# Performance work log

Hardware: AMD Instinct MI355X
Metric: run time of the kernel (lower is better)

## Reference

```python
import jax, jax.numpy as jnp
import numpy as np

B, Q, D, H, EF = 64, 300, 512, 8, 4
DH = D // H            # 64, per-head dim for scores
DV = (D * EF) // H     # 256, per-head value dim


def setup_inputs() -> dict:
    key = jax.random.key(0)
    ks = jax.random.split(key, 10)
    s = 0.02
    return {
        "query_feats": jax.random.normal(ks[0], (B, Q, D), jnp.float32),
        "bias": jax.random.normal(ks[1], (1, H, Q, Q), jnp.float32),
        "W_gen": jax.random.normal(ks[2], (D, D), jnp.float32) * s,
        "b_gen": jax.random.normal(ks[3], (D,), jnp.float32) * s,
        "W_val": jax.random.normal(ks[4], (D, D * EF), jnp.float32) * s,
        "b_val": jax.random.normal(ks[5], (D * EF,), jnp.float32) * s,
        "W_out": jax.random.normal(ks[6], (D * EF, D), jnp.float32) * s,
        "b_out": jax.random.normal(ks[7], (D,), jnp.float32) * s,
        "weight_bank": jnp.ones((1, H, Q, Q), jnp.float32) / np.sqrt(DH).astype(np.float32),
    }


def reference(query_feats, bias, W_gen, b_gen, W_val, b_val, W_out, b_out, weight_bank):
    bs, nq, d = query_feats.shape
    h = weight_bank.shape[1]
    # params_generator -> dynamic mixing matrix M: [bs, h, dh, nq]
    M = (query_feats @ W_gen + b_gen).reshape(bs, nq, h, -1).transpose(0, 2, 3, 1)
    # value: [bs, h, nq, dv]
    value = (query_feats @ W_val + b_val).reshape(bs, nq, h, -1).transpose(0, 2, 1, 3)
    # queries split per head: [bs, h, nq, dh]
    q = query_feats.reshape(bs, nq, h, -1).transpose(0, 2, 1, 3)
    # scores: [bs, h, nq, nq], scaled by learned weight bank + bias, GELU (exact), softmax
    scores = jnp.einsum('bhqd,bhdk->bhqk', q, M) * weight_bank + bias
    attn = jax.nn.softmax(jax.nn.gelu(scores, approximate=False), axis=-1)
    out = jnp.einsum('bhqk,bhkv->bhqv', attn, value)
    out = out.transpose(0, 2, 1, 3).reshape(bs, nq, -1)
    out = out @ W_out + b_out
    return out + query_feats
```

## Files before the change

### kernel.cpp

```cpp
#include <hip/hip_runtime.h>
#include <hip/hip_bf16.h>

typedef __attribute__((ext_vector_type(4))) float f32x4;
typedef __attribute__((ext_vector_type(8))) short s16x8;
typedef __attribute__((ext_vector_type(4))) short s16x4;

#define MFMA16(A, B, C) __builtin_amdgcn_mfma_f32_16x16x32_bf16((A), (B), (C), 0, 0, 0)

#define GLDS16(gsrc, ldst) __builtin_amdgcn_global_load_lds(                   \
    (const __attribute__((address_space(1))) void*)(gsrc),                    \
    (__attribute__((address_space(3))) void*)(ldst), 16, 0, 0)

__device__ __forceinline__ ushort f2bf(float f) {
    __hip_bfloat16 h = __float2bfloat16(f);
    return *reinterpret_cast<ushort*>(&h);
}

__device__ __forceinline__ float gelu_exact(float x) {
    float z = 0.70710678118f * x;
    float az = fabsf(z);
    float t = 1.0f / fmaf(0.3275911f, az, 1.0f);
    float poly = t * (0.254829592f + t * (-0.284496736f + t * (1.421413741f +
                 t * (-1.453152027f + t * 1.061405429f))));
    float e = __expf(-az * az);
    float erfv = copysignf(1.0f - poly * e, z);
    return 0.5f * x * (1.0f + erfv);
}

__global__ __launch_bounds__(256) void k_prep(const float* __restrict__ qf,
                                              ushort* __restrict__ qf_bf,
                                              const float* __restrict__ W_gen,
                                              const float* __restrict__ W_val,
                                              const float* __restrict__ W_out,
                                              ushort* __restrict__ WgvT,
                                              ushort* __restrict__ WoT,
                                              ushort* __restrict__ Vt) {
    __shared__ float tile[32][33];
    int blk = blockIdx.x;
    if (blk < 9600) {
        int i = (blk * 256 + threadIdx.x) * 4;
        float4 v = *(const float4*)(qf + i);
        ushort4 o;
        o.x = f2bf(v.x); o.y = f2bf(v.y); o.z = f2bf(v.z); o.w = f2bf(v.w);
        *(ushort4*)(qf_bf + i) = o;
        return;
    }
    blk -= 9600;
    if (blk >= 2304) {
        int i = ((blk - 2304) * 256 + threadIdx.x) * 8;
        int bh = i >> 13, within = i & 8191;
        s16x8 z = {0, 0, 0, 0, 0, 0, 0, 0};
        *(s16x8*)(Vt + ((size_t)bh * 10 + 9) * 8192 + within) = z;
        return;
    }
    const float* w; ushort* wt; int K, N, kx, ny;
    if (blk < 256)       { w = W_gen; wt = WgvT;             K = 512;  N = 512;
                           kx = blk & 15;          ny = blk >> 4; }
    else if (blk < 1280) { w = W_val; wt = WgvT + 512 * 512; K = 512;  N = 2048;
                           int b2 = blk - 256;  kx = b2 & 15; ny = b2 >> 4; }
    else                 { w = W_out; wt = WoT;              K = 2048; N = 512;
                           int b2 = blk - 1280; kx = b2 & 63; ny = b2 >> 6; }
    int k0 = kx * 32, n0 = ny * 32;
    int tx = threadIdx.x & 31, ty = threadIdx.x >> 5;
    #pragma unroll
    for (int i = ty; i < 32; i += 8)
        tile[i][tx] = w[(size_t)(k0 + i) * N + n0 + tx];
    __syncthreads();
    #pragma unroll
    for (int i = ty; i < 32; i += 8)
        wt[(size_t)(n0 + i) * K + k0 + tx] = f2bf(tile[tx][i]);
}

template <int OUT>
__global__ __launch_bounds__(512, 2) void k_gemm256(const ushort* __restrict__ A,
                                                    const ushort* __restrict__ BT,
                                                    const float* __restrict__ b1,
                                                    const float* __restrict__ b2,
                                                    void* __restrict__ o1,
                                                    void* __restrict__ o2,
                                                    int K, int GY) {
    __shared__ __align__(16) ushort As[2][256 * 64];
    __shared__ __align__(16) ushort Bs[2][256 * 64];
    int id = blockIdx.x;
    int xcd = id & 7, s = id >> 3;
    int mxl = s / GY, ny = s - mxl * GY;
    int mx = xcd * 10 + mxl;
    if (mx >= 75) return;
    int m0 = mx * 256, n0g = ny * 256;

    int t = threadIdx.x, l = t & 63, w = t >> 6;
    int wr = w >> 2, wc = w & 3;
    int lr = l & 15, lg = l >> 4;

    int rsrc[4], ksrc[4];
    #pragma unroll
    for (int c8 = 0; c8 < 4; ++c8) {
        int o = (c8 * 512 + t) * 16;
        int op = o ^ (((o >> 7) & 7) << 4);
        rsrc[c8] = op >> 7;
        ksrc[c8] = (op & 127) >> 1;
    }

    auto stage = [&](int kt, int buf) {
        int k0 = kt * 64;
        ushort* AsB = &As[buf][0];
        ushort* BsB = &Bs[buf][0];
        #pragma unroll
        for (int c8 = 0; c8 < 4; ++c8) {
            int dst = (c8 * 512 + w * 64) * 8;
            GLDS16(A  + (size_t)(m0 + rsrc[c8]) * K + k0 + ksrc[c8], AsB + dst);
            GLDS16(BT + (size_t)(n0g + rsrc[c8]) * K + k0 + ksrc[c8], BsB + dst);
        }
    };

    f32x4 acc[8][4];
    #pragma unroll
    for (int i = 0; i < 8; ++i)
        #pragma unroll
        for (int j = 0; j < 4; ++j)
            acc[i][j] = (f32x4){0.f, 0.f, 0.f, 0.f};

    int NT = K >> 6;
    stage(0, 0);
    stage(1, 1);

    for (int kt = 0; kt < NT; ++kt) {
        if (kt + 1 < NT) asm volatile("s_waitcnt vmcnt(8)" ::: "memory");
        else             asm volatile("s_waitcnt vmcnt(0)" ::: "memory");
        __builtin_amdgcn_s_barrier();

        int cur = kt & 1;
        const char* Ab = (const char*)&As[cur][0];
        const char* Bb = (const char*)&Bs[cur][0];
        #pragma unroll
        for (int ks = 0; ks < 2; ++ks) {
            int kb = (ks * 64 + lg * 16) ^ ((lr & 7) << 4);
            s16x8 af[8], bfv[4];
            #pragma unroll
            for (int rt = 0; rt < 8; ++rt)
                af[rt] = *(const s16x8*)(Ab + (wr * 128 + rt * 16 + lr) * 128 + kb);
            #pragma unroll
            for (int ct = 0; ct < 4; ++ct)
                bfv[ct] = *(const s16x8*)(Bb + (wc * 64 + ct * 16 + lr) * 128 + kb);
            #pragma unroll
            for (int rt = 0; rt < 8; ++rt)
                #pragma unroll
                for (int ct = 0; ct < 4; ++ct)
                    acc[rt][ct] = MFMA16(af[rt], bfv[ct], acc[rt][ct]);
        }

        __builtin_amdgcn_s_barrier();
        if (kt + 2 < NT) stage(kt + 2, cur);
    }

    if (OUT == 0) {
        if (n0g < 512) {
            ushort* G = (ushort*)o1;
            #pragma unroll
            for (int rt = 0; rt < 8; ++rt)
                #pragma unroll
                for (int ct = 0; ct < 4; ++ct) {
                    int col = n0g + wc * 64 + ct * 16 + lr;
                    float bv = b1[col];
                    #pragma unroll
                    for (int rr = 0; rr < 4; ++rr) {
                        int row = m0 + wr * 128 + rt * 16 + lg * 4 + rr;
                        G[(size_t)row * 512 + col] = f2bf(acc[rt][ct][rr] + bv);
                    }
                }
        } else {
            ushort* Vt = (ushort*)o2;
            #pragma unroll
            for (int rt = 0; rt < 8; ++rt) {
                int rl0 = m0 + wr * 128 + rt * 16 + lg * 4;
                int bb = rl0 / 300, key0 = rl0 - bb * 300;
                #pragma unroll
                for (int ct = 0; ct < 4; ++ct) {
                    int colv = n0g - 512 + wc * 64 + ct * 16 + lr;
                    float bv = b2[colv];
                    int hh = colv >> 8, v = colv & 255;
                    s16x4 pw;
                    #pragma unroll
                    for (int rr = 0; rr < 4; ++rr)
                        pw[rr] = (short)f2bf(acc[rt][ct][rr] + bv);
                    size_t addr = (((size_t)(bb * 8 + hh) * 10 + (key0 >> 5)) * 8192)
                                  + v * 32 + (key0 & 31);
                    *(s16x4*)(Vt + addr) = pw;
                }
            }
        }
    } else {
        float* out = (float*)o1;
        #pragma unroll
        for (int rt = 0; rt < 8; ++rt)
            #pragma unroll
            for (int ct = 0; ct < 4; ++ct) {
                int col = n0g + wc * 64 + ct * 16 + lr;
                float bv = b1[col];
                #pragma unroll
                for (int rr = 0; rr < 4; ++rr) {
                    int row = m0 + wr * 128 + rt * 16 + lg * 4 + rr;
                    size_t idx = (size_t)row * 512 + col;
                    out[idx] = acc[rt][ct][rr] + bv + b2[idx];
                }
            }
    }
}

__global__ __launch_bounds__(512, 4) void k_attn(const ushort* __restrict__ qf_bf,
                                                 const ushort* __restrict__ G_bf,
                                                 const ushort* __restrict__ Vt,
                                                 const float* __restrict__ wb,
                                                 const float* __restrict__ bias,
                                                 ushort* __restrict__ O) {
    __shared__ __align__(16) ushort P[64 * 320];
    __shared__ float partial[2][64];
    int id = blockIdx.x;
    int xcd = id & 7, s = id >> 3;
    int h = s / 40; int r2 = s - h * 40;
    int bi = r2 / 5, qt = r2 - bi * 5;
    int b = xcd * 8 + bi;

    int t = threadIdx.x, l = t & 63, w = t >> 6;
    int lr = l & 15, lg = l >> 4;
    int wq = w & 3, wk = w >> 2;

    auto p_addr = [&](int q, int k) -> ushort* {
        int byte = (q * 640 + k * 2) ^ ((q & 15) << 4);
        return (ushort*)((char*)P + byte);
    };

    int qr = min(qt * 64 + wq * 16 + lr, 299);
    const ushort* qp = qf_bf + ((size_t)(b * 300 + qr)) * 512 + h * 64 + lg * 8;
    s16x8 q0 = *(const s16x8*)(qp);
    s16x8 q1 = *(const s16x8*)(qp + 32);

    int qq = wq * 16 + lr;
    float ssum = 0.f;
    #pragma unroll
    for (int i = 0; i < 10; ++i) {
        int kt = wk * 10 + i;
        if (kt < 19) {
            int key = kt * 16 + lr;
            int kcl = min(key, 299);
            const ushort* gp = G_bf + ((size_t)(b * 300 + kcl)) * 512 + h * 64 + lg * 8;
            s16x8 g0 = *(const s16x8*)(gp);
            s16x8 g1 = *(const s16x8*)(gp + 32);
            f32x4 a = (f32x4){0.f, 0.f, 0.f, 0.f};
            a = MFMA16(g0, q0, a);
            a = MFMA16(g1, q1, a);
            int k0 = kt * 16 + lg * 4;
            int k0c = min(k0, 296);
            size_t bidx = ((size_t)h * 300 + qr) * 300 + k0c;
            float4 wv = *(const float4*)(wb + bidx);
            float4 bv = *(const float4*)(bias + bidx);
            bool vmask = (kt < 18) || (lg < 3);
            s16x4 pw;
            #pragma unroll
            for (int r = 0; r < 4; ++r) {
                float x = a[r] * (&wv.x)[r] + (&bv.x)[r];
                float p = vmask ? __expf(gelu_exact(x)) : 0.f;
                ssum += p;
                pw[r] = (short)f2bf(p);
            }
            *(s16x4*)p_addr(qq, k0) = pw;
        }
    }
    if (w >= 4) {
        int th = t - 256;
        *(s16x4*)p_addr(th >> 2, 304 + (th & 3) * 4) = (s16x4){0, 0, 0, 0};
    }

    ssum += __shfl_xor(ssum, 16);
    ssum += __shfl_xor(ssum, 32);
    if (lg == 0) partial[wk][qq] = ssum;

    __syncthreads();

    f32x4 acc[4][2];
    #pragma unroll
    for (int qg = 0; qg < 4; ++qg)
        #pragma unroll
        for (int nt = 0; nt < 2; ++nt)
            acc[qg][nt] = (f32x4){0.f, 0.f, 0.f, 0.f};

    const ushort* vbase = Vt + (size_t)(b * 8 + h) * 81920
                          + (size_t)(w * 32) * 32 + lg * 8;
    #pragma unroll
    for (int kc = 0; kc < 10; ++kc) {
        s16x8 vb[2], pa[4];
        #pragma unroll
        for (int nt = 0; nt < 2; ++nt)
            vb[nt] = *(const s16x8*)(vbase + (size_t)kc * 8192 + (nt * 16 + lr) * 32);
        #pragma unroll
        for (int qg = 0; qg < 4; ++qg)
            pa[qg] = *(const s16x8*)p_addr(qg * 16 + lr, kc * 32 + lg * 8);
        #pragma unroll
        for (int qg = 0; qg < 4; ++qg)
            #pragma unroll
            for (int nt = 0; nt < 2; ++nt)
                acc[qg][nt] = MFMA16(pa[qg], vb[nt], acc[qg][nt]);
    }

    #pragma unroll
    for (int qg = 0; qg < 4; ++qg)
        #pragma unroll
        for (int r = 0; r < 4; ++r) {
            int qloc = qg * 16 + lg * 4 + r;
            int q = qt * 64 + qloc;
            if (q < 300) {
                float iv = 1.0f / (partial[0][qloc] + partial[1][qloc]);
                #pragma unroll
                for (int nt = 0; nt < 2; ++nt) {
                    int v = w * 32 + nt * 16 + lr;
                    O[((size_t)(b * 300 + q)) * 2048 + h * 256 + v] =
                        f2bf(acc[qg][nt][r] * iv);
                }
            }
        }
}

extern "C" void kernel_launch(void* const* d_in, const int* in_sizes, int n_in,
                              void* d_out, int out_size, void* d_ws, size_t ws_size,
                              hipStream_t stream) {
    const float* qf    = (const float*)d_in[0];
    const float* bias  = (const float*)d_in[1];
    const float* W_gen = (const float*)d_in[2];
    const float* b_gen = (const float*)d_in[3];
    const float* W_val = (const float*)d_in[4];
    const float* b_val = (const float*)d_in[5];
    const float* W_out = (const float*)d_in[6];
    const float* b_out = (const float*)d_in[7];
    const float* wb    = (const float*)d_in[8];
    float* out = (float*)d_out;

    char* ws = (char*)d_ws;
    ushort* qf_bf = (ushort*)(ws);
    ushort* G_bf  = (ushort*)(ws + 19660800);
    ushort* Vt    = (ushort*)(ws + 39321600);
    ushort* O_bf  = (ushort*)(ws + 123207680);
    ushort* WgvT  = (ushort*)(ws + 201850880);
    ushort* WoT   = (ushort*)(ws + 204472320);

    k_prep<<<dim3(13952), dim3(256), 0, stream>>>(qf, qf_bf, W_gen, W_val, W_out,
                                                  WgvT, WoT, Vt);

    k_gemm256<0><<<dim3(800), dim3(512), 0, stream>>>(qf_bf, WgvT, b_gen, b_val,
                                                      G_bf, Vt, 512, 10);

    k_attn<<<dim3(2560), dim3(512), 0, stream>>>(qf_bf, G_bf, Vt, wb, bias, O_bf);

    k_gemm256<2><<<dim3(160), dim3(512), 0, stream>>>(O_bf, WoT, b_out, qf,
                                                      out, nullptr, 2048, 2);
}
```

Measured before the change: 297.5 us.

## Pack weight bank and bias into transposed bf16 pairs, approximate GELU, trim key padding

Weight bank and bias are transposed and packed into one 32-bit word per element (two bf16 values) in the prep kernel, so the attention kernel reads one packed value per score instead of two fp32 float4 loads. The exact erf-based GELU is replaced with a sigmoid-style tanh approximation built on exp2 and rcp intrinsics, which cuts ALU work per score. The V layout shrinks the last key chunk to 16 keys, so the PV loop runs 9 full chunks plus one half chunk and less zero padding is written and read. The packed reads are strided by 300 elements per key, which may coalesce worse, and the GELU approximation plus bf16 weight and bias change numerical accuracy.

```diff
diff --git a/kernel.cpp b/kernel.cpp
--- a/kernel.cpp
+++ b/kernel.cpp
@@ -16,15 +16,12 @@
     return *reinterpret_cast<ushort*>(&h);
 }
 
-__device__ __forceinline__ float gelu_exact(float x) {
-    float z = 0.70710678118f * x;
-    float az = fabsf(z);
-    float t = 1.0f / fmaf(0.3275911f, az, 1.0f);
-    float poly = t * (0.254829592f + t * (-0.284496736f + t * (1.421413741f +
-                 t * (-1.453152027f + t * 1.061405429f))));
-    float e = __expf(-az * az);
-    float erfv = copysignf(1.0f - poly * e, z);
-    return 0.5f * x * (1.0f + erfv);
+__device__ __forceinline__ float exp_gelu(float x) {
+    float u = x * x;
+    float m = fmaf(-0.1029439065f, u, -2.3022154392f);
+    float e2 = __builtin_amdgcn_exp2f(x * m);
+    float g = x * __builtin_amdgcn_rcpf(1.0f + e2);
+    return __expf(g);
 }
 
 __global__ __launch_bounds__(256) void k_prep(const float* __restrict__ qf,
@@ -32,11 +29,16 @@
                                               const float* __restrict__ W_gen,
                                               const float* __restrict__ W_val,
                                               const float* __restrict__ W_out,
+                                              const float* __restrict__ wb,
+                                              const float* __restrict__ bias,
                                               ushort* __restrict__ WgvT,
                                               ushort* __restrict__ WoT,
+                                              unsigned int* __restrict__ wbbT,
                                               ushort* __restrict__ Vt) {
     __shared__ float tile[32][33];
+    __shared__ float tb[32][33];
     int blk = blockIdx.x;
+    int tx = threadIdx.x & 31, ty = threadIdx.x >> 5;
     if (blk < 9600) {
         int i = (blk * 256 + threadIdx.x) * 4;
         float4 v = *(const float4*)(qf + i);
@@ -46,29 +48,50 @@
         return;
     }
     blk -= 9600;
-    if (blk >= 2304) {
-        int i = ((blk - 2304) * 256 + threadIdx.x) * 8;
-        int bh = i >> 13, within = i & 8191;
-        s16x8 z = {0, 0, 0, 0, 0, 0, 0, 0};
-        *(s16x8*)(Vt + ((size_t)bh * 10 + 9) * 8192 + within) = z;
+    if (blk < 2304) {
+        const float* w; ushort* wt; int K, N, kx, ny;
+        if (blk < 256)       { w = W_gen; wt = WgvT;             K = 512;  N = 512;
+                               kx = blk & 15;          ny = blk >> 4; }
+        else if (blk < 1280) { w = W_val; wt = WgvT + 512 * 512; K = 512;  N = 2048;
+                               int b2 = blk - 256;  kx = b2 & 15; ny = b2 >> 4; }
+        else                 { w = W_out; wt = WoT;              K = 2048; N = 512;
+                               int b2 = blk - 1280; kx = b2 & 63; ny = b2 >> 6; }
+        int k0 = kx * 32, n0 = ny * 32;
+        #pragma unroll
+        for (int i = ty; i < 32; i += 8)
+            tile[i][tx] = w[(size_t)(k0 + i) * N + n0 + tx];
+        __syncthreads();
+        #pragma unroll
+        for (int i = ty; i < 32; i += 8)
+            wt[(size_t)(n0 + i) * K + k0 + tx] = f2bf(tile[tx][i]);
         return;
     }
-    const float* w; ushort* wt; int K, N, kx, ny;
-    if (blk < 256)       { w = W_gen; wt = WgvT;             K = 512;  N = 512;
-                           kx = blk & 15;          ny = blk >> 4; }
-    else if (blk < 1280) { w = W_val; wt = WgvT + 512 * 512; K = 512;  N = 2048;
-                           int b2 = blk - 256;  kx = b2 & 15; ny = b2 >> 4; }
-    else                 { w = W_out; wt = WoT;              K = 2048; N = 512;
-                           int b2 = blk - 1280; kx = b2 & 63; ny = b2 >> 6; }
-    int k0 = kx * 32, n0 = ny * 32;
-    int tx = threadIdx.x & 31, ty = threadIdx.x >> 5;
-    #pragma unroll
-    for (int i = ty; i < 32; i += 8)
-        tile[i][tx] = w[(size_t)(k0 + i) * N + n0 + tx];
-    __syncthreads();
-    #pragma unroll
-    for (int i = ty; i < 32; i += 8)
-        wt[(size_t)(n0 + i) * K + k0 + tx] = f2bf(tile[tx][i]);
+    blk -= 2304;
+    if (blk < 800) {
+        int h = blk / 100, rem = blk - h * 100;
+        int kx = rem / 10, qx = rem - kx * 10;
+        int k0 = kx * 32, q0 = qx * 32;
+        #pragma unroll
+        for (int i = ty; i < 32; i += 8)
+            if (q0 + i < 300 && k0 + tx < 300) {
+                size_t si = ((size_t)h * 300 + q0 + i) * 300 + k0 + tx;
+                tile[i][tx] = wb[si];
+                tb[i][tx]   = bias[si];
+            }
+        __syncthreads();
+        #pragma unroll
+        for (int i = ty; i < 32; i += 8)
+            if (k0 + i < 300 && q0 + tx < 300) {
+                unsigned int pk = (unsigned int)f2bf(tile[tx][i])
+                                | ((unsigned int)f2bf(tb[tx][i]) << 16);
+                wbbT[((size_t)h * 300 + k0 + i) * 300 + q0 + tx] = pk;
+            }
+        return;
+    }
+    blk -= 800;
+    int tid = blk * 256 + threadIdx.x;
+    int bh = tid >> 8, v = tid & 255;
+    *(s16x4*)(Vt + (size_t)bh * 77824 + 73728 + v * 16 + 12) = (s16x4){0, 0, 0, 0};
 }
 
 template <int OUT>
@@ -183,8 +206,10 @@
                     #pragma unroll
                     for (int rr = 0; rr < 4; ++rr)
                         pw[rr] = (short)f2bf(acc[rt][ct][rr] + bv);
-                    size_t addr = (((size_t)(bb * 8 + hh) * 10 + (key0 >> 5)) * 8192)
-                                  + v * 32 + (key0 & 31);
+                    size_t bhb = (size_t)(bb * 8 + hh) * 77824;
+                    size_t addr = (key0 < 288)
+                        ? bhb + (size_t)(key0 >> 5) * 8192 + v * 32 + (key0 & 31)
+                        : bhb + 73728 + v * 16 + (key0 - 288);
                     *(s16x4*)(Vt + addr) = pw;
                 }
             }
@@ -210,8 +235,7 @@
 __global__ __launch_bounds__(512, 4) void k_attn(const ushort* __restrict__ qf_bf,
                                                  const ushort* __restrict__ G_bf,
                                                  const ushort* __restrict__ Vt,
-                                                 const float* __restrict__ wb,
-                                                 const float* __restrict__ bias,
+                                                 const unsigned int* __restrict__ wbb,
                                                  ushort* __restrict__ O) {
     __shared__ __align__(16) ushort P[64 * 320];
     __shared__ float partial[2][64];
@@ -235,40 +259,56 @@
     s16x8 q0 = *(const s16x8*)(qp);
     s16x8 q1 = *(const s16x8*)(qp + 32);
 
+    const unsigned int* wbbq = wbb + (size_t)h * 90000 + qr;
+
     int qq = wq * 16 + lr;
     float ssum = 0.f;
-    #pragma unroll
-    for (int i = 0; i < 10; ++i) {
-        int kt = wk * 10 + i;
-        if (kt < 19) {
-            int key = kt * 16 + lr;
-            int kcl = min(key, 299);
-            const ushort* gp = G_bf + ((size_t)(b * 300 + kcl)) * 512 + h * 64 + lg * 8;
-            s16x8 g0 = *(const s16x8*)(gp);
-            s16x8 g1 = *(const s16x8*)(gp + 32);
-            f32x4 a = (f32x4){0.f, 0.f, 0.f, 0.f};
-            a = MFMA16(g0, q0, a);
-            a = MFMA16(g1, q1, a);
-            int k0 = kt * 16 + lg * 4;
-            int k0c = min(k0, 296);
-            size_t bidx = ((size_t)h * 300 + qr) * 300 + k0c;
-            float4 wv = *(const float4*)(wb + bidx);
-            float4 bv = *(const float4*)(bias + bidx);
-            bool vmask = (kt < 18) || (lg < 3);
-            s16x4 pw;
-            #pragma unroll
-            for (int r = 0; r < 4; ++r) {
-                float x = a[r] * (&wv.x)[r] + (&bv.x)[r];
-                float p = vmask ? __expf(gelu_exact(x)) : 0.f;
-                ssum += p;
-                pw[r] = (short)f2bf(p);
-            }
-            *(s16x4*)p_addr(qq, k0) = pw;
-        }
-    }
-    if (w >= 4) {
-        int th = t - 256;
-        *(s16x4*)p_addr(th >> 2, 304 + (th & 3) * 4) = (s16x4){0, 0, 0, 0};
+    int ktlo = wk * 10, kthi = min(ktlo + 10, 18);
+    for (int kt = ktlo; kt < kthi; ++kt) {
+        int key = kt * 16 + lr;
+        const ushort* gp = G_bf + ((size_t)(b * 300 + key)) * 512 + h * 64 + lg * 8;
+        s16x8 g0 = *(const s16x8*)(gp);
+        s16x8 g1 = *(const s16x8*)(gp + 32);
+        f32x4 a = (f32x4){0.f, 0.f, 0.f, 0.f};
+        a = MFMA16(g0, q0, a);
+        a = MFMA16(g1, q1, a);
+        int kbase = kt * 16 + lg * 4;
+        s16x4 pw;
+        #pragma unroll
+        for (int r = 0; r < 4; ++r) {
+            unsigned int u = wbbq[(size_t)(kbase + r) * 300];
+            float wv = __builtin_bit_cast(float, u << 16);
+            float bv = __builtin_bit_cast(float, u & 0xffff0000u);
+            float x = fmaf(a[r], wv, bv);
+            float p = exp_gelu(x);
+            ssum += p;
+            pw[r] = (short)f2bf(p);
+        }
+        *(s16x4*)p_addr(qq, kbase) = pw;
+    }
+    if (wk == 1) {
+        int key = 288 + lr;
+        int kcl = min(key, 299);
+        const ushort* gp = G_bf + ((size_t)(b * 300 + kcl)) * 512 + h * 64 + lg * 8;
+        s16x8 g0 = *(const s16x8*)(gp);
+        s16x8 g1 = *(const s16x8*)(gp + 32);
+        f32x4 a = (f32x4){0.f, 0.f, 0.f, 0.f};
+        a = MFMA16(g0, q0, a);
+        a = MFMA16(g1, q1, a);
+        int kbase = 288 + lg * 4;
+        s16x4 pw;
+        #pragma unroll
+        for (int r = 0; r < 4; ++r) {
+            int kc2 = min(kbase + r, 299);
+            unsigned int u = wbbq[(size_t)kc2 * 300];
+            float wv = __builtin_bit_cast(float, u << 16);
+            float bv = __builtin_bit_cast(float, u & 0xffff0000u);
+            float x = fmaf(a[r], wv, bv);
+            float p = (lg < 3) ? exp_gelu(x) : 0.f;
+            ssum += p;
+            pw[r] = (short)f2bf(p);
+        }
+        *(s16x4*)p_addr(qq, kbase) = pw;
     }
 
     ssum += __shfl_xor(ssum, 16);
@@ -284,10 +324,10 @@
         for (int nt = 0; nt < 2; ++nt)
             acc[qg][nt] = (f32x4){0.f, 0.f, 0.f, 0.f};
 
-    const ushort* vbase = Vt + (size_t)(b * 8 + h) * 81920
-                          + (size_t)(w * 32) * 32 + lg * 8;
+    size_t bhb = (size_t)(b * 8 + h) * 77824;
+    const ushort* vbase = Vt + bhb + (size_t)(w * 32) * 32 + lg * 8;
     #pragma unroll
-    for (int kc = 0; kc < 10; ++kc) {
+    for (int kc = 0; kc < 9; ++kc) {
         s16x8 vb[2], pa[4];
         #pragma unroll
         for (int nt = 0; nt < 2; ++nt)
@@ -295,6 +335,28 @@
         #pragma unroll
         for (int qg = 0; qg < 4; ++qg)
             pa[qg] = *(const s16x8*)p_addr(qg * 16 + lr, kc * 32 + lg * 8);
+        #pragma unroll
+        for (int qg = 0; qg < 4; ++qg)
+            #pragma unroll
+            for (int nt = 0; nt < 2; ++nt)
+                acc[qg][nt] = MFMA16(pa[qg], vb[nt], acc[qg][nt]);
+    }
+    {
+        s16x8 vb[2], pa[4];
+        const ushort* c9 = Vt + bhb + 73728 + (size_t)(w * 32) * 16 + lg * 8;
+        if (lg < 2) {
+            #pragma unroll
+            for (int nt = 0; nt < 2; ++nt)
+                vb[nt] = *(const s16x8*)(c9 + (nt * 16 + lr) * 16);
+            #pragma unroll
+            for (int qg = 0; qg < 4; ++qg)
+                pa[qg] = *(const s16x8*)p_addr(qg * 16 + lr, 288 + lg * 8);
+        } else {
+            #pragma unroll
+            for (int nt = 0; nt < 2; ++nt) vb[nt] = (s16x8){0,0,0,0,0,0,0,0};
+            #pragma unroll
+            for (int qg = 0; qg < 4; ++qg) pa[qg] = (s16x8){0,0,0,0,0,0,0,0};
+        }
         #pragma unroll
         for (int qg = 0; qg < 4; ++qg)
             #pragma unroll
@@ -338,17 +400,18 @@
     ushort* qf_bf = (ushort*)(ws);
     ushort* G_bf  = (ushort*)(ws + 19660800);
     ushort* Vt    = (ushort*)(ws + 39321600);
-    ushort* O_bf  = (ushort*)(ws + 123207680);
-    ushort* WgvT  = (ushort*)(ws + 201850880);
-    ushort* WoT   = (ushort*)(ws + 204472320);
-
-    k_prep<<<dim3(13952), dim3(256), 0, stream>>>(qf, qf_bf, W_gen, W_val, W_out,
-                                                  WgvT, WoT, Vt);
+    ushort* O_bf  = (ushort*)(ws + 119013376);
+    ushort* WgvT  = (ushort*)(ws + 197656576);
+    ushort* WoT   = (ushort*)(ws + 200278016);
+    unsigned int* wbbT = (unsigned int*)(ws + 202375168);
+
+    k_prep<<<dim3(13216), dim3(256), 0, stream>>>(qf, qf_bf, W_gen, W_val, W_out,
+                                                  wb, bias, WgvT, WoT, wbbT, Vt);
 
     k_gemm256<0><<<dim3(800), dim3(512), 0, stream>>>(qf_bf, WgvT, b_gen, b_val,
                                                       G_bf, Vt, 512, 10);
 
-    k_attn<<<dim3(2560), dim3(512), 0, stream>>>(qf_bf, G_bf, Vt, wb, bias, O_bf);
+    k_attn<<<dim3(2560), dim3(512), 0, stream>>>(qf_bf, G_bf, Vt, wbbT, O_bf);
 
     k_gemm256<2><<<dim3(160), dim3(512), 0, stream>>>(O_bf, WoT, b_out, qf,
                                                       out, nullptr, 2048, 2);
```

Result: faster. 273.5 us (-8.1%).
